# Performance work log

Hardware: AMD Instinct MI355X
Metric: run time of the kernel (lower is better)

The kernel has to match this reference:

```python
import jax, jax.numpy as jnp
import numpy as np

B, T, D = 1, 2048, 2048
H, G, HD = 16, 4, 128          # num_heads, num_kv_groups, head_dim
GS = H // G                    # group_size
EPS = 1e-6


def rmsnorm(x, w):
    return x * jax.lax.rsqrt(jnp.mean(x * x, axis=-1, keepdims=True) + EPS) * w


def apply_rope(x, cos, sin, offset=0):
    # x: [B, heads, T, HD]; cos/sin: [max_seq, HD]
    t = x.shape[2]
    c = cos[offset:offset + t][None, None]  # [1,1,T,HD]
    s = sin[offset:offset + t][None, None]
    x1, x2 = x[..., : HD // 2], x[..., HD // 2:]
    rot = jnp.concatenate([-x2, x1], axis=-1)
    return x * c + rot * s


def setup_inputs() -> dict:
    key = jax.random.key(0)
    ks = jax.random.split(key, 8)
    x = jax.random.normal(ks[0], (B, T, D), dtype=jnp.float32)
    # causal mask: True = masked out
    mask = jnp.triu(jnp.ones((T, T), dtype=bool), k=1)[None, None]
    # RoPE tables (theta=10000), duplicated-halves layout
    inv_freq = 1.0 / (10000.0 ** (jnp.arange(0, HD, 2, dtype=jnp.float32) / HD))
    angles = jnp.arange(T, dtype=jnp.float32)[:, None] * inv_freq[None, :]  # [T, HD/2]
    angles = jnp.concatenate([angles, angles], axis=-1)                     # [T, HD]
    cos, sin = jnp.cos(angles), jnp.sin(angles)
    sc = 0.02
    Wq = jax.random.normal(ks[1], (H * HD, D), dtype=jnp.float32) * sc
    Wk = jax.random.normal(ks[2], (G * HD, D), dtype=jnp.float32) * sc
    Wv = jax.random.normal(ks[3], (G * HD, D), dtype=jnp.float32) * sc
    Wo = jax.random.normal(ks[4], (D, H * HD), dtype=jnp.float32) * sc
    q_norm_w = jnp.ones((H * HD,), dtype=jnp.float32)
    k_norm_w = jnp.ones((G * HD,), dtype=jnp.float32)
    return {"x": x, "mask": mask, "cos": cos, "sin": sin,
            "Wq": Wq, "Wk": Wk, "Wv": Wv, "Wo": Wo,
            "q_norm_w": q_norm_w, "k_norm_w": k_norm_w}


def reference(x, mask, cos, sin, Wq, Wk, Wv, Wo, q_norm_w, k_norm_w):
    b, t, _ = x.shape
    q = rmsnorm(x @ Wq.T, q_norm_w)   # [B,T,H*HD]
    k = rmsnorm(x @ Wk.T, k_norm_w)   # [B,T,G*HD]
    v = x @ Wv.T                      # [B,T,G*HD]
    q = q.reshape(b, t, H, HD).transpose(0, 2, 1, 3)   # [B,H,T,HD]
    k = k.reshape(b, t, G, HD).transpose(0, 2, 1, 3)   # [B,G,T,HD]
    v = v.reshape(b, t, G, HD).transpose(0, 2, 1, 3)
    q = apply_rope(q, cos, sin, offset=0)
    k = apply_rope(k, cos, sin, offset=0)
    # GQA: repeat_interleave KV heads to match query heads
    k = jnp.repeat(k, GS, axis=1)     # [B,H,T,HD]
    vr = jnp.repeat(v, GS, axis=1)
    q = q * (HD ** -0.5)
    scores = jnp.einsum('bhqd,bhkd->bhqk', q, k)        # [B,H,T,T]
    scores = jnp.where(mask, -jnp.inf, scores)
    attn = jax.nn.softmax(scores, axis=-1)
    ctx = jnp.einsum('bhqk,bhkd->bhqd', attn, vr)
    ctx = ctx.transpose(0, 2, 1, 3).reshape(b, t, H * HD)
    return ctx @ Wo.T                                   # [B,T,D]
```

## Files before the change

### kernel.cpp

```cpp
#include <hip/hip_runtime.h>

#define T_SEQ 2048
#define DMODEL 2048
#define NHEADS 16
#define NKV 4
#define HDIM 128
#define KVDIM (NKV*HDIM)
#define QKVN (DMODEL + 2*KVDIM)

typedef __bf16 bf16x8 __attribute__((ext_vector_type(8)));
typedef float f32x4 __attribute__((ext_vector_type(4)));
typedef unsigned short us8 __attribute__((ext_vector_type(8)));
typedef unsigned short ushort_t;

__device__ __forceinline__ ushort_t f2b(float f) {
    union { float f; unsigned u; } c; c.f = f;
    unsigned r = c.u + 0x7FFFu + ((c.u >> 16) & 1u);
    return (ushort_t)(r >> 16);
}
__device__ __forceinline__ ushort_t f2b_rn(float f) {
    union { __bf16 h; ushort_t u; } c; c.h = (__bf16)f; return c.u;
}
__device__ __forceinline__ float b2f(ushort_t b) {
    union { unsigned u; float f; } c; c.u = ((unsigned)b) << 16; return c.f;
}

#define GLDS(g, l) __builtin_amdgcn_global_load_lds( \
    (const __attribute__((address_space(1))) void*)(g), \
    (__attribute__((address_space(3))) void*)(l), 16, 0, 0)

__global__ __launch_bounds__(256) void cvt5_kernel(
    const float* __restrict__ s0, ushort_t* __restrict__ d0, int c0,
    const float* __restrict__ s1, ushort_t* __restrict__ d1, int c1,
    const float* __restrict__ s2, ushort_t* __restrict__ d2, int c2,
    const float* __restrict__ s3, ushort_t* __restrict__ d3, int c3,
    const float* __restrict__ s4, ushort_t* __restrict__ d4, int c4)
{
    int u = blockIdx.x * 256 + threadIdx.x;
    const float* s; ushort_t* d; int off;
    if      (u < c0) { s = s0; d = d0; off = u; }
    else if (u < c1) { s = s1; d = d1; off = u - c0; }
    else if (u < c2) { s = s2; d = d2; off = u - c1; }
    else if (u < c3) { s = s3; d = d3; off = u - c2; }
    else if (u < c4) { s = s4; d = d4; off = u - c3; }
    else return;
    const float4 v = *(const float4*)(s + off * 4);
    ushort4 o = make_ushort4(f2b(v.x), f2b(v.y), f2b(v.z), f2b(v.w));
    *(ushort4*)(d + off * 4) = o;
}

template<int MODE>
__global__ __launch_bounds__(256) void gemm_bt(
    const ushort_t* __restrict__ A, const ushort_t* __restrict__ B,
    ushort_t* __restrict__ Cb, float* __restrict__ Cf, ushort_t* __restrict__ VT,
    int M, int N, int K)
{
    __shared__ ushort_t As[128 * 64];
    __shared__ ushort_t Bs[128 * 64];
    const int tid = threadIdx.x;
    const int lane = tid & 63;
    const int wv = tid >> 6;
    const int wr = wv >> 1, wc = wv & 1;
    const int lrow = lane & 15, lhi = lane >> 4;
    const int m0 = blockIdx.y * 128, n0 = blockIdx.x * 128;

    f32x4 acc[4][4];
#pragma unroll
    for (int i = 0; i < 4; i++)
#pragma unroll
        for (int j = 0; j < 4; j++) acc[i][j] = f32x4{0.f, 0.f, 0.f, 0.f};

    const int srow = tid >> 3;
    const int scol = (tid & 7) * 8;

    for (int kt = 0; kt < K; kt += 64) {
        if (kt) __syncthreads();
#pragma unroll
        for (int r = 0; r < 4; ++r) {
            int row = srow + r * 32;
            GLDS(A + (size_t)(m0 + row) * K + kt + scol, As + row * 64 + scol);
            GLDS(B + (size_t)(n0 + row) * K + kt + scol, Bs + row * 64 + scol);
        }
        __syncthreads();
#pragma unroll
        for (int kk = 0; kk < 2; ++kk) {
            bf16x8 af[4], bfr[4];
#pragma unroll
            for (int i = 0; i < 4; i++)
                af[i] = *(const bf16x8*)(As + (wr * 64 + i * 16 + lrow) * 64 + kk * 32 + lhi * 8);
#pragma unroll
            for (int j = 0; j < 4; j++)
                bfr[j] = *(const bf16x8*)(Bs + (wc * 64 + j * 16 + lrow) * 64 + kk * 32 + lhi * 8);
#pragma unroll
            for (int i = 0; i < 4; i++)
#pragma unroll
                for (int j = 0; j < 4; j++)
                    acc[i][j] = __builtin_amdgcn_mfma_f32_16x16x32_bf16(af[i], bfr[j], acc[i][j], 0, 0, 0);
        }
    }
    if (MODE == 2 && n0 >= DMODEL + KVDIM) {
#pragma unroll
        for (int i = 0; i < 4; i++)
#pragma unroll
            for (int j = 0; j < 4; j++) {
                int col = n0 + wc * 64 + j * 16 + lrow - (DMODEL + KVDIM);
                int row0 = m0 + wr * 64 + i * 16 + lhi * 4;
                ushort4 pk = make_ushort4(f2b(acc[i][j][0]), f2b(acc[i][j][1]),
                                          f2b(acc[i][j][2]), f2b(acc[i][j][3]));
                *(ushort4*)(VT + (size_t)col * T_SEQ + row0) = pk;
            }
    } else {
#pragma unroll
        for (int i = 0; i < 4; i++)
#pragma unroll
            for (int j = 0; j < 4; j++)
#pragma unroll
                for (int e = 0; e < 4; e++) {
                    int row = m0 + wr * 64 + i * 16 + lhi * 4 + e;
                    int col = n0 + wc * 64 + j * 16 + lrow;
                    if (MODE == 1) Cf[(size_t)row * N + col] = acc[i][j][e];
                    else           Cb[(size_t)row * N + col] = f2b(acc[i][j][e]);
                }
    }
}

template<int DROW>
__device__ __forceinline__ void norm_rope_body(
    const ushort_t* __restrict__ src, int sld, int scol,
    const float* __restrict__ w,
    const float* __restrict__ cosT, const float* __restrict__ sinT,
    ushort_t* __restrict__ dst, int dld, float oscale,
    float* rowbuf, float* red)
{
    constexpr int PER = DROW / 256;
    const int tid = threadIdx.x;
    const int t = blockIdx.x;
    const ushort_t* rp = src + (size_t)t * sld + scol;
    const int e0 = tid * PER;

    float vals[PER];
    if constexpr (PER == 8) {
        us8 u = *(const us8*)(rp + e0);
#pragma unroll
        for (int p = 0; p < PER; p++) vals[p] = b2f(u[p]);
    } else {
        ushort2 u = *(const ushort2*)(rp + e0);
        vals[0] = b2f(u.x); vals[1] = b2f(u.y);
    }
    float ss = 0.f;
#pragma unroll
    for (int p = 0; p < PER; p++) { ss += vals[p] * vals[p]; rowbuf[e0 + p] = vals[p]; }
#pragma unroll
    for (int o = 32; o; o >>= 1) ss += __shfl_down(ss, o);
    if ((tid & 63) == 0) red[tid >> 6] = ss;
    __syncthreads();
    float rn = rsqrtf((red[0] + red[1] + red[2] + red[3]) / (float)DROW + 1e-6f);
#pragma unroll
    for (int p = 0; p < PER; p++) {
        int e = e0 + p, r = e & 127;
        float c = cosT[t * HDIM + r], s = sinT[t * HDIM + r];
        int pe = (r < 64) ? e + 64 : e - 64;
        float self = rowbuf[e] * rn * w[e];
        float part = rowbuf[pe] * rn * w[pe];
        float o = (r < 64) ? (self * c - part * s) : (self * c + part * s);
        dst[(size_t)t * dld + e] = f2b(o * oscale);
    }
}

__global__ __launch_bounds__(256) void norm_rope_qk(
    const ushort_t* __restrict__ qkv,
    const float* __restrict__ qw, const float* __restrict__ kw,
    const float* __restrict__ cosT, const float* __restrict__ sinT,
    ushort_t* __restrict__ qb, ushort_t* __restrict__ kb)
{
    __shared__ float rowbuf[DMODEL];
    __shared__ float red[4];
    if (blockIdx.y == 0)
        norm_rope_body<DMODEL>(qkv, QKVN, 0, qw, cosT, sinT, qb, DMODEL,
                               0.08838834764831843f, rowbuf, red);
    else
        norm_rope_body<KVDIM>(qkv, QKVN, DMODEL, kw, cosT, sinT, kb, KVDIM,
                              1.0f, rowbuf, red);
}

__global__ __launch_bounds__(256) void fattn(
    const ushort_t* __restrict__ Q,
    const ushort_t* __restrict__ Kb,
    const ushort_t* __restrict__ VT,
    ushort_t* __restrict__ ctx)
{
    __shared__ ushort_t Ks[2][64 * 128];
    __shared__ ushort_t Vt[2][128 * 64];
    __shared__ ushort_t Pw[4][16 * 64];
    const int tid = threadIdx.x, lane = tid & 63, wv = tid >> 6;
    const int lrow = lane & 15, lhi = lane >> 4;
    const int h = blockIdx.x;
    const int qt = 31 - (int)blockIdx.y;
    const int g = h >> 2;
    const int q0 = qt * 64;

    const int srK = tid >> 4, scK = tid & 15;
    const int srV = tid >> 3, scV = tid & 7;

    bf16x8 qf[4];
    {
        int qr = q0 + wv * 16 + lrow;
#pragma unroll
        for (int ks = 0; ks < 4; ks++)
            qf[ks] = *(const bf16x8*)(Q + (size_t)qr * DMODEL + h * HDIM + ks * 32 + lhi * 8);
    }
    f32x4 of[8];
#pragma unroll
    for (int f = 0; f < 8; f++) of[f] = f32x4{0.f, 0.f, 0.f, 0.f};
    float m_[4], l_[4];
#pragma unroll
    for (int j = 0; j < 4; j++) { m_[j] = -1e30f; l_[j] = 0.f; }
    int myrow[4];
#pragma unroll
    for (int j = 0; j < 4; j++) myrow[j] = q0 + wv * 16 + lhi * 4 + j;

    auto stage = [&](int kt, int b) {
        const int k0 = kt * 64;
#pragma unroll
        for (int r = 0; r < 4; r++) {
            int row = srK + r * 16;
            int c = scK ^ (row & 7);
            GLDS(Kb + (size_t)(k0 + row) * KVDIM + g * HDIM + c * 8,
                 Ks[b] + row * 128 + scK * 8);
        }
#pragma unroll
        for (int r = 0; r < 4; r++) {
            int row = srV + r * 32;
            int c = scV ^ (row & 7);
            GLDS(VT + (size_t)(g * HDIM + row) * T_SEQ + k0 + c * 8,
                 Vt[b] + row * 64 + scV * 8);
        }
    };

    stage(0, 0);
    __syncthreads();
    int buf = 0;

    for (int kt = 0; kt <= qt; ++kt) {
        if (kt < qt) stage(kt + 1, buf ^ 1);
        const ushort_t* KsB = Ks[buf];
        const ushort_t* VtB = Vt[buf];
        const int k0 = kt * 64;

        f32x4 sf[4];
#pragma unroll
        for (int nf = 0; nf < 4; nf++) sf[nf] = f32x4{0.f, 0.f, 0.f, 0.f};
#pragma unroll
        for (int ks = 0; ks < 4; ks++) {
#pragma unroll
            for (int nf = 0; nf < 4; nf++) {
                bf16x8 kf = *(const bf16x8*)(KsB + (nf * 16 + lrow) * 128 +
                                             (((ks * 4 + lhi) ^ (lrow & 7)) << 3));
                sf[nf] = __builtin_amdgcn_mfma_f32_16x16x32_bf16(qf[ks], kf, sf[nf], 0, 0, 0);
            }
        }
#pragma unroll
        for (int nf = 0; nf < 4; nf++) {
            int key = k0 + nf * 16 + lrow;
#pragma unroll
            for (int j = 0; j < 4; j++)
                if (key > myrow[j]) sf[nf][j] = -1e30f;
        }
        float mx[4];
#pragma unroll
        for (int j = 0; j < 4; j++) {
            float m2 = fmaxf(fmaxf(sf[0][j], sf[1][j]), fmaxf(sf[2][j], sf[3][j]));
#pragma unroll
            for (int o = 1; o < 16; o <<= 1) m2 = fmaxf(m2, __shfl_xor(m2, o));
            mx[j] = m2;
        }
        float need = fmaxf(fmaxf(mx[0] - m_[0], mx[1] - m_[1]),
                           fmaxf(mx[2] - m_[2], mx[3] - m_[3]));
        if (!__all(need <= 8.0f)) {
#pragma unroll
            for (int j = 0; j < 4; j++) {
                float mn = fmaxf(m_[j], mx[j]);
                float sc = __expf(m_[j] - mn);
                m_[j] = mn;
                l_[j] *= sc;
#pragma unroll
                for (int f = 0; f < 8; f++) of[f][j] *= sc;
            }
        }
        float pf[4][4];
#pragma unroll
        for (int nf = 0; nf < 4; nf++)
#pragma unroll
            for (int j = 0; j < 4; j++) pf[nf][j] = __expf(sf[nf][j] - m_[j]);
#pragma unroll
        for (int j = 0; j < 4; j++)
            l_[j] += (pf[0][j] + pf[1][j]) + (pf[2][j] + pf[3][j]);
#pragma unroll
        for (int nf = 0; nf < 4; nf++)
#pragma unroll
            for (int j = 0; j < 4; j++) {
                int q = lhi * 4 + j;
                int cb = (nf * 16 + lrow) * 2;
                int cbp = cb ^ ((q & 7) << 4);
                Pw[wv][q * 64 + (cbp >> 1)] = f2b_rn(pf[nf][j]);
            }
#pragma unroll
        for (int k2 = 0; k2 < 2; k2++) {
            bf16x8 pa = *(const bf16x8*)(Pw[wv] + lrow * 64 +
                                         (((k2 * 4 + lhi) ^ (lrow & 7)) << 3));
#pragma unroll
            for (int f = 0; f < 8; f++) {
                bf16x8 vf = *(const bf16x8*)(VtB + (f * 16 + lrow) * 64 +
                                             (((k2 * 4 + lhi) ^ (lrow & 7)) << 3));
                of[f] = __builtin_amdgcn_mfma_f32_16x16x32_bf16(pa, vf, of[f], 0, 0, 0);
            }
        }
        __syncthreads();
        buf ^= 1;
    }
#pragma unroll
    for (int j = 0; j < 4; j++) {
#pragma unroll
        for (int o = 1; o < 16; o <<= 1) l_[j] += __shfl_xor(l_[j], o);
    }
#pragma unroll
    for (int f = 0; f < 8; f++)
#pragma unroll
        for (int j = 0; j < 4; j++) {
            float o = of[f][j] / l_[j];
            ctx[(size_t)myrow[j] * DMODEL + h * HDIM + f * 16 + lrow] = f2b_rn(o);
        }
}

extern "C" void kernel_launch(void* const* d_in, const int* in_sizes, int n_in,
                              void* d_out, int out_size, void* d_ws, size_t ws_size,
                              hipStream_t stream)
{
    const float* x    = (const float*)d_in[0];
    const float* cosT = (const float*)d_in[2];
    const float* sinT = (const float*)d_in[3];
    const float* Wq   = (const float*)d_in[4];
    const float* Wk   = (const float*)d_in[5];
    const float* Wv   = (const float*)d_in[6];
    const float* Wo   = (const float*)d_in[7];
    const float* qw   = (const float*)d_in[8];
    const float* kw   = (const float*)d_in[9];
    float* out = (float*)d_out;

    char* ws = (char*)d_ws;
    size_t off = 0;
    auto alloc = [&](size_t bytes) -> char* {
        char* p = ws + off; off += (bytes + 255) & ~(size_t)255; return p;
    };
    ushort_t* xb    = (ushort_t*)alloc((size_t)T_SEQ * DMODEL * 2);
    ushort_t* wqkvb = (ushort_t*)alloc((size_t)QKVN * DMODEL * 2);
    ushort_t* wob   = (ushort_t*)alloc((size_t)DMODEL * DMODEL * 2);
    ushort_t* qkvb  = (ushort_t*)alloc((size_t)T_SEQ * QKVN * 2);
    ushort_t* qb    = (ushort_t*)alloc((size_t)T_SEQ * DMODEL * 2);
    ushort_t* kb    = (ushort_t*)alloc((size_t)T_SEQ * KVDIM * 2);
    ushort_t* ctxb  = (ushort_t*)alloc((size_t)T_SEQ * DMODEL * 2);
    ushort_t* vtb   = (ushort_t*)alloc((size_t)KVDIM * T_SEQ * 2);

    const int n_x  = T_SEQ * DMODEL / 4;
    const int n_wq = DMODEL * DMODEL / 4;
    const int n_wk = KVDIM * DMODEL / 4;
    const int n_wv = KVDIM * DMODEL / 4;
    const int n_wo = DMODEL * DMODEL / 4;
    const int c0 = n_x, c1 = c0 + n_wq, c2 = c1 + n_wk, c3 = c2 + n_wv, c4 = c3 + n_wo;
    cvt5_kernel<<<dim3((c4 + 255) / 256), dim3(256), 0, stream>>>(
        x,  xb, c0,
        Wq, wqkvb, c1,
        Wk, wqkvb + (size_t)DMODEL * DMODEL, c2,
        Wv, wqkvb + (size_t)(DMODEL + KVDIM) * DMODEL, c3,
        Wo, wob, c4);

    gemm_bt<2><<<dim3(QKVN / 128, T_SEQ / 128), dim3(256), 0, stream>>>(
        xb, wqkvb, qkvb, nullptr, vtb, T_SEQ, QKVN, DMODEL);

    norm_rope_qk<<<dim3(T_SEQ, 2), dim3(256), 0, stream>>>(
        qkvb, qw, kw, cosT, sinT, qb, kb);

    fattn<<<dim3(NHEADS, 32), dim3(256), 0, stream>>>(qb, kb, vtb, ctxb);

    gemm_bt<1><<<dim3(DMODEL / 128, T_SEQ / 128), dim3(256), 0, stream>>>(
        ctxb, wob, nullptr, out, nullptr, T_SEQ, DMODEL, DMODEL);
}
```

Measured before the change: 292.3 us.

## Shrink flash-attention tiles to 32x32 with 2-wave blocks and transposed S MFMA

Reworks the attention kernel to use 32-query blocks of two waves and 32-key tiles, doubling the grid to 1024 blocks for better CU occupancy and load balance on the causal triangle. The QK^T MFMA is transposed (K as A operand) so each lane owns one query row, which removes most cross-lane max and sum shuffles and lets P be written to LDS as packed 4-element vectors with a new swizzle. Smaller tiles mean less reuse of K/V loads per block and more loop iterations with syncs, in exchange for higher parallelism.

```diff
diff --git a/kernel.cpp b/kernel.cpp
--- a/kernel.cpp
+++ b/kernel.cpp
@@ -183,24 +183,26 @@
                               1.0f, rowbuf, red);
 }
 
-__global__ __launch_bounds__(256) void fattn(
+__global__ __launch_bounds__(128, 2) void fattn(
     const ushort_t* __restrict__ Q,
     const ushort_t* __restrict__ Kb,
     const ushort_t* __restrict__ VT,
     ushort_t* __restrict__ ctx)
 {
-    __shared__ ushort_t Ks[2][64 * 128];
-    __shared__ ushort_t Vt[2][128 * 64];
-    __shared__ ushort_t Pw[4][16 * 64];
+    __shared__ ushort_t Ks[2][32 * 128];
+    __shared__ ushort_t Vt[2][128 * 32];
+    __shared__ ushort_t Pw[2][16 * 32];
     const int tid = threadIdx.x, lane = tid & 63, wv = tid >> 6;
     const int lrow = lane & 15, lhi = lane >> 4;
     const int h = blockIdx.x;
-    const int qt = 31 - (int)blockIdx.y;
+    const int qt = 63 - (int)blockIdx.y;
     const int g = h >> 2;
-    const int q0 = qt * 64;
+    const int q0 = qt * 32;
+    const int sw = (lrow >> 1) & 3;
+    const int kswz = lrow & 7;
 
     const int srK = tid >> 4, scK = tid & 15;
-    const int srV = tid >> 3, scV = tid & 7;
+    const int srV = tid >> 2, scV = tid & 3;
 
     bf16x8 qf[4];
     {
@@ -212,28 +214,22 @@
     f32x4 of[8];
 #pragma unroll
     for (int f = 0; f < 8; f++) of[f] = f32x4{0.f, 0.f, 0.f, 0.f};
-    float m_[4], l_[4];
-#pragma unroll
-    for (int j = 0; j < 4; j++) { m_[j] = -1e30f; l_[j] = 0.f; }
-    int myrow[4];
-#pragma unroll
-    for (int j = 0; j < 4; j++) myrow[j] = q0 + wv * 16 + lhi * 4 + j;
+    float m_ = -1e30f, l_ = 0.f;
+    const int myq = q0 + wv * 16 + lrow;
 
     auto stage = [&](int kt, int b) {
-        const int k0 = kt * 64;
+        const int k0 = kt * 32;
 #pragma unroll
         for (int r = 0; r < 4; r++) {
-            int row = srK + r * 16;
-            int c = scK ^ (row & 7);
-            GLDS(Kb + (size_t)(k0 + row) * KVDIM + g * HDIM + c * 8,
-                 Ks[b] + row * 128 + scK * 8);
+            int row = r * 8 + srK;
+            GLDS(Kb + (size_t)(k0 + row) * KVDIM + g * HDIM + ((scK ^ (row & 7)) << 3),
+                 Ks[b] + row * 128 + (scK << 3));
         }
 #pragma unroll
         for (int r = 0; r < 4; r++) {
-            int row = srV + r * 32;
-            int c = scV ^ (row & 7);
-            GLDS(VT + (size_t)(g * HDIM + row) * T_SEQ + k0 + c * 8,
-                 Vt[b] + row * 64 + scV * 8);
+            int row = r * 32 + srV;
+            GLDS(VT + (size_t)(g * HDIM + row) * T_SEQ + k0 + ((scV ^ ((row >> 1) & 3)) << 3),
+                 Vt[b] + row * 32 + (scV << 3));
         }
     };
 
@@ -245,90 +241,77 @@
         if (kt < qt) stage(kt + 1, buf ^ 1);
         const ushort_t* KsB = Ks[buf];
         const ushort_t* VtB = Vt[buf];
-        const int k0 = kt * 64;
-
-        f32x4 sf[4];
-#pragma unroll
-        for (int nf = 0; nf < 4; nf++) sf[nf] = f32x4{0.f, 0.f, 0.f, 0.f};
+        const int k0 = kt * 32;
+
+        f32x4 sf[2];
+        sf[0] = f32x4{0.f, 0.f, 0.f, 0.f};
+        sf[1] = f32x4{0.f, 0.f, 0.f, 0.f};
 #pragma unroll
         for (int ks = 0; ks < 4; ks++) {
 #pragma unroll
-            for (int nf = 0; nf < 4; nf++) {
+            for (int nf = 0; nf < 2; nf++) {
                 bf16x8 kf = *(const bf16x8*)(KsB + (nf * 16 + lrow) * 128 +
-                                             (((ks * 4 + lhi) ^ (lrow & 7)) << 3));
-                sf[nf] = __builtin_amdgcn_mfma_f32_16x16x32_bf16(qf[ks], kf, sf[nf], 0, 0, 0);
+                                             (((ks * 4 + lhi) ^ kswz) << 3));
+                sf[nf] = __builtin_amdgcn_mfma_f32_16x16x32_bf16(kf, qf[ks], sf[nf], 0, 0, 0);
             }
         }
 #pragma unroll
-        for (int nf = 0; nf < 4; nf++) {
-            int key = k0 + nf * 16 + lrow;
+        for (int nf = 0; nf < 2; nf++)
 #pragma unroll
             for (int j = 0; j < 4; j++)
-                if (key > myrow[j]) sf[nf][j] = -1e30f;
-        }
-        float mx[4];
-#pragma unroll
-        for (int j = 0; j < 4; j++) {
-            float m2 = fmaxf(fmaxf(sf[0][j], sf[1][j]), fmaxf(sf[2][j], sf[3][j]));
-#pragma unroll
-            for (int o = 1; o < 16; o <<= 1) m2 = fmaxf(m2, __shfl_xor(m2, o));
-            mx[j] = m2;
-        }
-        float need = fmaxf(fmaxf(mx[0] - m_[0], mx[1] - m_[1]),
-                           fmaxf(mx[2] - m_[2], mx[3] - m_[3]));
-        if (!__all(need <= 8.0f)) {
+                if (k0 + nf * 16 + lhi * 4 + j > myq) sf[nf][j] = -1e30f;
+        float mx = fmaxf(fmaxf(fmaxf(sf[0][0], sf[0][1]), fmaxf(sf[0][2], sf[0][3])),
+                         fmaxf(fmaxf(sf[1][0], sf[1][1]), fmaxf(sf[1][2], sf[1][3])));
+        mx = fmaxf(mx, __shfl_xor(mx, 16));
+        mx = fmaxf(mx, __shfl_xor(mx, 32));
+        if (!__all(mx - m_ <= 8.0f)) {
+            float mn = fmaxf(m_, mx);
+            float sc = __expf(m_ - mn);
+            m_ = mn;
+            l_ *= sc;
+            float scb[4];
+#pragma unroll
+            for (int j = 0; j < 4; j++) scb[j] = __shfl(sc, lhi * 4 + j);
+#pragma unroll
+            for (int f = 0; f < 8; f++)
+#pragma unroll
+                for (int j = 0; j < 4; j++) of[f][j] *= scb[j];
+        }
+        float pf[2][4];
+#pragma unroll
+        for (int nf = 0; nf < 2; nf++)
 #pragma unroll
             for (int j = 0; j < 4; j++) {
-                float mn = fmaxf(m_[j], mx[j]);
-                float sc = __expf(m_[j] - mn);
-                m_[j] = mn;
-                l_[j] *= sc;
-#pragma unroll
-                for (int f = 0; f < 8; f++) of[f][j] *= sc;
+                pf[nf][j] = __expf(sf[nf][j] - m_);
+                l_ += pf[nf][j];
             }
-        }
-        float pf[4][4];
-#pragma unroll
-        for (int nf = 0; nf < 4; nf++)
-#pragma unroll
-            for (int j = 0; j < 4; j++) pf[nf][j] = __expf(sf[nf][j] - m_[j]);
-#pragma unroll
-        for (int j = 0; j < 4; j++)
-            l_[j] += (pf[0][j] + pf[1][j]) + (pf[2][j] + pf[3][j]);
-#pragma unroll
-        for (int nf = 0; nf < 4; nf++)
-#pragma unroll
-            for (int j = 0; j < 4; j++) {
-                int q = lhi * 4 + j;
-                int cb = (nf * 16 + lrow) * 2;
-                int cbp = cb ^ ((q & 7) << 4);
-                Pw[wv][q * 64 + (cbp >> 1)] = f2b_rn(pf[nf][j]);
-            }
-#pragma unroll
-        for (int k2 = 0; k2 < 2; k2++) {
-            bf16x8 pa = *(const bf16x8*)(Pw[wv] + lrow * 64 +
-                                         (((k2 * 4 + lhi) ^ (lrow & 7)) << 3));
-#pragma unroll
-            for (int f = 0; f < 8; f++) {
-                bf16x8 vf = *(const bf16x8*)(VtB + (f * 16 + lrow) * 64 +
-                                             (((k2 * 4 + lhi) ^ (lrow & 7)) << 3));
-                of[f] = __builtin_amdgcn_mfma_f32_16x16x32_bf16(pa, vf, of[f], 0, 0, 0);
-            }
+#pragma unroll
+        for (int nf = 0; nf < 2; nf++) {
+            ushort4 pk = make_ushort4(f2b_rn(pf[nf][0]), f2b_rn(pf[nf][1]),
+                                      f2b_rn(pf[nf][2]), f2b_rn(pf[nf][3]));
+            int u = 2 * nf + (lhi >> 1);
+            *(ushort4*)(Pw[wv] + lrow * 32 + ((u ^ sw) << 3) + ((lhi & 1) << 2)) = pk;
+        }
+        bf16x8 pa = *(const bf16x8*)(Pw[wv] + lrow * 32 + ((lhi ^ sw) << 3));
+#pragma unroll
+        for (int f = 0; f < 8; f++) {
+            bf16x8 vf = *(const bf16x8*)(VtB + (f * 16 + lrow) * 32 + ((lhi ^ sw) << 3));
+            of[f] = __builtin_amdgcn_mfma_f32_16x16x32_bf16(pa, vf, of[f], 0, 0, 0);
         }
         __syncthreads();
         buf ^= 1;
     }
-#pragma unroll
-    for (int j = 0; j < 4; j++) {
-#pragma unroll
-        for (int o = 1; o < 16; o <<= 1) l_[j] += __shfl_xor(l_[j], o);
-    }
+    l_ += __shfl_xor(l_, 16);
+    l_ += __shfl_xor(l_, 32);
+    float lb[4];
+#pragma unroll
+    for (int j = 0; j < 4; j++) lb[j] = __shfl(l_, lhi * 4 + j);
 #pragma unroll
     for (int f = 0; f < 8; f++)
 #pragma unroll
         for (int j = 0; j < 4; j++) {
-            float o = of[f][j] / l_[j];
-            ctx[(size_t)myrow[j] * DMODEL + h * HDIM + f * 16 + lrow] = f2b_rn(o);
+            int qrow = q0 + wv * 16 + lhi * 4 + j;
+            ctx[(size_t)qrow * DMODEL + h * HDIM + f * 16 + lrow] = f2b_rn(of[f][j] / lb[j]);
         }
 }
 
@@ -380,7 +363,7 @@
     norm_rope_qk<<<dim3(T_SEQ, 2), dim3(256), 0, stream>>>(
         qkvb, qw, kw, cosT, sinT, qb, kb);
 
-    fattn<<<dim3(NHEADS, 32), dim3(256), 0, stream>>>(qb, kb, vtb, ctxb);
+    fattn<<<dim3(NHEADS, 64), dim3(128), 0, stream>>>(qb, kb, vtb, ctxb);
 
     gemm_bt<1><<<dim3(DMODEL / 128, T_SEQ / 128), dim3(256), 0, stream>>>(
         ctxb, wob, nullptr, out, nullptr, T_SEQ, DMODEL, DMODEL);
```

After: 296.9 us. No clear change (+1.5%).
